# Optimization experiments

Hardware: AMD Instinct MI355X
Metric: run time of the kernel (lower is better)

Reference implementation:

```python
import jax, jax.numpy as jnp
import numpy as np

EMBED_DIM = 1024
NUM_HEADS = 16
HEAD_DIM = EMBED_DIM // NUM_HEADS


def setup_inputs() -> dict:
    key = jax.random.key(0)
    ks = jax.random.split(key, 11)
    Lq, N, E = 4096, 4, EMBED_DIM
    Lk = 4096
    s = 1.0 / np.sqrt(E)
    return {
        "q": jax.random.normal(ks[0], (Lq, N, E), jnp.float32),
        "k": jax.random.normal(ks[1], (Lk, N, E), jnp.float32),
        "v": jax.random.normal(ks[2], (Lk, N, E), jnp.float32),
        "Wq": jax.random.normal(ks[3], (E, E), jnp.float32) * s,
        "bq": jnp.zeros((E,), jnp.float32),
        "Wk": jax.random.normal(ks[4], (E, E), jnp.float32) * s,
        "bk": jnp.zeros((E,), jnp.float32),
        "Wv": jax.random.normal(ks[5], (E, E), jnp.float32) * s,
        "bv": jnp.zeros((E,), jnp.float32),
        "Wo": jax.random.normal(ks[6], (E, E), jnp.float32) * s,
        "bo": jnp.zeros((E,), jnp.float32),
    }


def reference(q, k, v, Wq, bq, Wk, bk, Wv, bv, Wo, bo):
    Lq, N, E = q.shape
    Lk = k.shape[0]
    H, D = NUM_HEADS, HEAD_DIM
    # Linear projections (torch Linear: x @ W.T + b)
    qp = q @ Wq.T + bq  # [Lq, N, E]
    kp = k @ Wk.T + bk  # [Lk, N, E]
    vp = v @ Wv.T + bv  # [Lk, N, E]
    # Split heads -> [N, H, L, D]
    qh = qp.reshape(Lq, N, H, D).transpose(1, 2, 0, 3)
    kh = kp.reshape(Lk, N, H, D).transpose(1, 2, 0, 3)
    vh = vp.reshape(Lk, N, H, D).transpose(1, 2, 0, 3)
    # Efficient (linear) attention
    kh = jax.nn.softmax(kh, axis=-2)            # softmax over sequence (L)
    v_prime = jnp.einsum('nhld,nhle->nhde', kh, vh)  # [N,H,D,D]
    qh = jax.nn.softmax(qh, axis=-1)            # softmax over feature (D)
    attn = jnp.einsum('nhld,nhde->nhle', qh, v_prime)  # [N,H,Lq,D]
    out = attn.transpose(2, 0, 1, 3).reshape(Lq, N, E)
    out = out @ Wo.T + bo
    return out
```

## Files before the change

kernel.cpp:

```cpp
#include <hip/hip_runtime.h>

typedef unsigned short u16;
typedef short s8v __attribute__((ext_vector_type(8)));
typedef float f4v __attribute__((ext_vector_type(4)));

#define D_LQ 4096
#define D_N 4
#define D_E 1024
#define D_M 16384
#define D_COLS 4096

__device__ __forceinline__ u16 f2b(float f) {
  unsigned u = __float_as_uint(f);
  return (u16)((u + 0x7FFFu + ((u >> 16) & 1u)) >> 16);
}
__device__ __forceinline__ float b2f(u16 x) {
  return __uint_as_float(((unsigned)x) << 16);
}
__device__ __forceinline__ s8v cvt8(float4 a, float4 b) {
  s8v o;
  o[0] = (short)f2b(a.x); o[1] = (short)f2b(a.y);
  o[2] = (short)f2b(a.z); o[3] = (short)f2b(a.w);
  o[4] = (short)f2b(b.x); o[5] = (short)f2b(b.y);
  o[6] = (short)f2b(b.z); o[7] = (short)f2b(b.w);
  return o;
}
__device__ __forceinline__ void gl_lds16(const void* g, void* l) {
  __builtin_amdgcn_global_load_lds(
      (const __attribute__((address_space(1))) void*)g,
      (__attribute__((address_space(3))) void*)l, 16, 0, 0);
}

__global__ void cvt_bf16(const float* __restrict__ in, u16* __restrict__ out, long n8) {
  long i = (long)blockIdx.x * 256 + threadIdx.x;
  if (i >= n8) return;
  const float4* p = (const float4*)in + 2 * i;
  float4 a = p[0], b = p[1];
  *(s8v*)(out + i * 8) = cvt8(a, b);
}

__global__ void cvt_w4(const float* __restrict__ W0, const float* __restrict__ W1,
                       const float* __restrict__ W2, const float* __restrict__ W3,
                       u16* __restrict__ O0, u16* __restrict__ O1,
                       u16* __restrict__ O2, u16* __restrict__ O3) {
  long i = (long)blockIdx.x * 256 + threadIdx.x;
  int w = blockIdx.y;
  const float* W = (w == 0) ? W0 : (w == 1) ? W1 : (w == 2) ? W2 : W3;
  u16* O = (w == 0) ? O0 : (w == 1) ? O1 : (w == 2) ? O2 : O3;
  const float4* p = (const float4*)W + 2 * i;
  float4 a = p[0], b = p[1];
  *(s8v*)(O + i * 8) = cvt8(a, b);
}

__global__ __launch_bounds__(256)
void gemm_bfb(const u16* __restrict__ A, const u16* __restrict__ B,
              const float* __restrict__ bias, u16* __restrict__ C) {
  __shared__ u16 As[128 * 32];
  __shared__ u16 Bs[128 * 32];
  const int tid = threadIdx.x;
  const int lane = tid & 63, r15 = lane & 15, khi = lane >> 4;
  const int wave = tid >> 6, wm = wave >> 1, wn = wave & 1;
  const int wg = blockIdx.y * 8 + blockIdx.x;
  const int xcd = wg & 7, j = wg >> 3;
  const int by = xcd * 16 + (j >> 3);
  const int bx = j & 7;
  f4v acc[4][4] = {};
  const u16* a0 = A + (long)(by * 128 + (tid >> 2)) * D_E + (tid & 3) * 8;
  const u16* b0 = B + (long)(bx * 128 + (tid >> 2)) * D_E + (tid & 3) * 8;
  const long rstep = (long)64 * D_E;
  u16* lA = As + tid * 8;
  u16* lB = Bs + tid * 8;
  for (int kt = 0; kt < D_E; kt += 32) {
    __syncthreads();
    gl_lds16(a0 + kt, lA);
    gl_lds16(a0 + rstep + kt, lA + 2048);
    gl_lds16(b0 + kt, lB);
    gl_lds16(b0 + rstep + kt, lB + 2048);
    __syncthreads();
    s8v af[4], bf[4];
#pragma unroll
    for (int m = 0; m < 4; m++)
      af[m] = *(const s8v*)(As + (wm * 64 + m * 16 + r15) * 32 + khi * 8);
#pragma unroll
    for (int n = 0; n < 4; n++)
      bf[n] = *(const s8v*)(Bs + (wn * 64 + n * 16 + r15) * 32 + khi * 8);
#pragma unroll
    for (int m = 0; m < 4; m++)
#pragma unroll
      for (int n = 0; n < 4; n++)
        acc[m][n] = __builtin_amdgcn_mfma_f32_16x16x32_bf16(af[m], bf[n], acc[m][n], 0, 0, 0);
  }
#pragma unroll
  for (int m = 0; m < 4; m++) {
    const int row = by * 128 + wm * 64 + m * 16 + khi * 4;
#pragma unroll
    for (int n = 0; n < 4; n++) {
      const int col = bx * 128 + wn * 64 + n * 16 + r15;
      const float bb = bias[col];
#pragma unroll
      for (int j2 = 0; j2 < 4; j2++)
        C[(long)(row + j2) * D_E + col] = f2b(acc[m][n][j2] + bb);
    }
  }
}

__global__ __launch_bounds__(256)
void gemm_bf_qsm(const u16* __restrict__ A, const u16* __restrict__ B,
                 const float* __restrict__ bias, u16* __restrict__ Csm) {
  __shared__ u16 As[128 * 32];
  __shared__ u16 Bs[128 * 32];
  const int tid = threadIdx.x;
  const int lane = tid & 63, r15 = lane & 15, khi = lane >> 4;
  const int wave = tid >> 6, wm = wave >> 1, wn = wave & 1;
  const int wg = blockIdx.y * 8 + blockIdx.x;
  const int xcd = wg & 7, j = wg >> 3;
  const int by = xcd * 16 + (j >> 3);
  const int bx = j & 7;
  f4v acc[4][4] = {};
  const u16* a0 = A + (long)(by * 128 + (tid >> 2)) * D_E + (tid & 3) * 8;
  const u16* b0 = B + (long)(bx * 128 + (tid >> 2)) * D_E + (tid & 3) * 8;
  const long rstep = (long)64 * D_E;
  u16* lA = As + tid * 8;
  u16* lB = Bs + tid * 8;
  for (int kt = 0; kt < D_E; kt += 32) {
    __syncthreads();
    gl_lds16(a0 + kt, lA);
    gl_lds16(a0 + rstep + kt, lA + 2048);
    gl_lds16(b0 + kt, lB);
    gl_lds16(b0 + rstep + kt, lB + 2048);
    __syncthreads();
    s8v af[4], bf[4];
#pragma unroll
    for (int m = 0; m < 4; m++)
      af[m] = *(const s8v*)(As + (wm * 64 + m * 16 + r15) * 32 + khi * 8);
#pragma unroll
    for (int n = 0; n < 4; n++)
      bf[n] = *(const s8v*)(Bs + (wn * 64 + n * 16 + r15) * 32 + khi * 8);
#pragma unroll
    for (int m = 0; m < 4; m++)
#pragma unroll
      for (int n = 0; n < 4; n++)
        acc[m][n] = __builtin_amdgcn_mfma_f32_16x16x32_bf16(af[m], bf[n], acc[m][n], 0, 0, 0);
  }
  const int colb = bx * 128 + wn * 64;
  float bb[4];
#pragma unroll
  for (int n = 0; n < 4; n++) bb[n] = bias[colb + n * 16 + r15];
#pragma unroll
  for (int m = 0; m < 4; m++) {
    const int row = by * 128 + wm * 64 + m * 16 + khi * 4;
#pragma unroll
    for (int j2 = 0; j2 < 4; j2++) {
      float e[4], s = 0.f;
#pragma unroll
      for (int n = 0; n < 4; n++) { e[n] = __expf(acc[m][n][j2] + bb[n]); s += e[n]; }
      s += __shfl_xor(s, 1);
      s += __shfl_xor(s, 2);
      s += __shfl_xor(s, 4);
      s += __shfl_xor(s, 8);
      float rs = 1.f / s;
#pragma unroll
      for (int n = 0; n < 4; n++)
        Csm[(long)(row + j2) * D_E + colb + n * 16 + r15] = f2b(e[n] * rs);
    }
  }
}

__global__ void k_sum(const u16* __restrict__ kb, float* __restrict__ psum) {
  int col = blockIdx.x * 256 + threadIdx.x;
  const u16* p = kb + (long)blockIdx.y * 64 * D_COLS + col;
  float s = 0.f;
  for (int l = 0; l < 64; l++) s += __expf(b2f(p[(long)l * D_COLS]));
  psum[blockIdx.y * D_COLS + col] = s;
}

__global__ void k_combine(const float* __restrict__ psum, float* __restrict__ crs) {
  int col = blockIdx.x * 256 + threadIdx.x;
  float s = 0.f;
  for (int i = 0; i < 64; i++) s += psum[i * D_COLS + col];
  crs[col] = 1.f / s;
}

__global__ __launch_bounds__(256)
void vprime_part(const u16* __restrict__ kw, const u16* __restrict__ vp,
                 const float* __restrict__ crs, float* __restrict__ part) {
  __shared__ float Ks[64 * 64];
  __shared__ float Vs[64 * 64];
  __shared__ float crS[64];
  int g = blockIdx.x, lc = blockIdx.y;
  int n = g >> 4, h = g & 15;
  int tid = threadIdx.x;
  int dt = (tid >> 4) * 4, et = (tid & 15) * 4;
  int r = tid >> 2, c16 = (tid & 3) * 16;
  if (tid < 64) crS[tid] = crs[n * D_E + h * 64 + tid];
  float acc[4][4] = {};
  long base = (long)lc * 512 * D_COLS + n * D_E + h * 64;
  for (int ch = 0; ch < 8; ch++) {
    long off = base + (long)(ch * 64 + r) * D_COLS + c16;
    __syncthreads();
#pragma unroll
    for (int qq = 0; qq < 16; qq++) {
      Ks[r * 64 + c16 + qq] = __expf(b2f(kw[off + qq])) * crS[c16 + qq];
      Vs[r * 64 + c16 + qq] = b2f(vp[off + qq]);
    }
    __syncthreads();
    for (int l = 0; l < 64; l++) {
      float kf[4], vf[4];
#pragma unroll
      for (int i = 0; i < 4; i++) { kf[i] = Ks[l * 64 + dt + i]; vf[i] = Vs[l * 64 + et + i]; }
#pragma unroll
      for (int i = 0; i < 4; i++)
#pragma unroll
        for (int j = 0; j < 4; j++) acc[i][j] += kf[i] * vf[j];
    }
  }
#pragma unroll
  for (int i = 0; i < 4; i++)
#pragma unroll
    for (int j = 0; j < 4; j++)
      part[(((long)lc * 64 + g) * 64 + (dt + i)) * 64 + et + j] = acc[i][j];
}

__global__ void vprime_red(const float* __restrict__ part, u16* __restrict__ vpb) {
  long id = (long)blockIdx.x * 256 + threadIdx.x;
  float s = 0.f;
  for (int lc = 0; lc < 8; lc++) s += part[(long)lc * 64 * 4096 + id];
  vpb[id] = f2b(s);
}

__global__ __launch_bounds__(256)
void u_mfma(const u16* __restrict__ Wob, const u16* __restrict__ vpb,
            u16* __restrict__ Ub) {
  __shared__ u16 Qs[128 * 64];
  __shared__ u16 Ps[64 * 64];
  const int ot = blockIdx.x, g = blockIdx.y;
  const int nb = g >> 4, h = g & 15;
  const int tid = threadIdx.x;
  const int lane = tid & 63, r15 = lane & 15, khi = lane >> 4;
  const int w = tid >> 6;
#pragma unroll
  for (int it = 0; it < 4; it++) {
    int c = it * 256 + tid;
    int row = c >> 3, cb = (c & 7) * 16;
    int swz = cb ^ ((row & 7) << 4);
    gl_lds16(Wob + (long)(ot * 128 + row) * D_E + h * 64 + (swz >> 1), Qs + c * 8);
  }
#pragma unroll
  for (int it = 0; it < 2; it++) {
    int c = it * 256 + tid;
    int row = c >> 3, cb = (c & 7) * 16;
    int swz = cb ^ ((row & 7) << 4);
    gl_lds16(vpb + ((long)g << 12) + row * 64 + (swz >> 1), Ps + c * 8);
  }
  __syncthreads();
  f4v acc[2][4] = {};
#pragma unroll
  for (int ks = 0; ks < 2; ks++) {
    s8v af[2], bf[4];
#pragma unroll
    for (int mf = 0; mf < 2; mf++) {
      int row = w * 32 + mf * 16 + r15;
      int boff = row * 128 + ((ks * 64 + khi * 16) ^ ((row & 7) << 4));
      af[mf] = *(const s8v*)((const char*)Qs + boff);
    }
#pragma unroll
    for (int nf = 0; nf < 4; nf++) {
      int row = nf * 16 + r15;
      int boff = row * 128 + ((ks * 64 + khi * 16) ^ ((row & 7) << 4));
      bf[nf] = *(const s8v*)((const char*)Ps + boff);
    }
#pragma unroll
    for (int mf = 0; mf < 2; mf++)
#pragma unroll
      for (int nf = 0; nf < 4; nf++)
        acc[mf][nf] = __builtin_amdgcn_mfma_f32_16x16x32_bf16(af[mf], bf[nf], acc[mf][nf], 0, 0, 0);
  }
#pragma unroll
  for (int mf = 0; mf < 2; mf++) {
#pragma unroll
    for (int nf = 0; nf < 4; nf++) {
#pragma unroll
      for (int j = 0; j < 4; j++) {
        int o = ot * 128 + w * 32 + mf * 16 + khi * 4 + j;
        int d = nf * 16 + r15;
        Ub[((long)nb * 1024 + o) * 1024 + h * 64 + d] = f2b(acc[mf][nf][j]);
      }
    }
  }
}

__global__ __launch_bounds__(256)
void gemm_out(const u16* __restrict__ Aq, const u16* __restrict__ Bu,
              const float* __restrict__ bias, float* __restrict__ C) {
  __shared__ u16 As[128 * 32];
  __shared__ u16 Bs[128 * 32];
  const int tid = threadIdx.x;
  const int lane = tid & 63, r15 = lane & 15, khi = lane >> 4;
  const int wave = tid >> 6, wm = wave >> 1, wn = wave & 1;
  const int n = blockIdx.z;
  const int wg = blockIdx.y * 8 + blockIdx.x;
  const int xcd = wg & 7, j = wg >> 3;
  const int by = xcd * 4 + (j >> 3);
  const int bx = j & 7;
  f4v acc[4][4] = {};
  const u16* a0 = Aq + ((long)(by * 128 + (tid >> 2)) * 4 + n) * D_E + (tid & 3) * 8;
  const u16* b0 = Bu + ((long)n * 1024 + bx * 128 + (tid >> 2)) * D_E + (tid & 3) * 8;
  const long rstepA = (long)64 * 4 * D_E;
  const long rstepB = (long)64 * D_E;
  u16* lA = As + tid * 8;
  u16* lB = Bs + tid * 8;
  for (int kt = 0; kt < D_E; kt += 32) {
    __syncthreads();
    gl_lds16(a0 + kt, lA);
    gl_lds16(a0 + rstepA + kt, lA + 2048);
    gl_lds16(b0 + kt, lB);
    gl_lds16(b0 + rstepB + kt, lB + 2048);
    __syncthreads();
    s8v af[4], bf[4];
#pragma unroll
    for (int m = 0; m < 4; m++)
      af[m] = *(const s8v*)(As + (wm * 64 + m * 16 + r15) * 32 + khi * 8);
#pragma unroll
    for (int nn = 0; nn < 4; nn++)
      bf[nn] = *(const s8v*)(Bs + (wn * 64 + nn * 16 + r15) * 32 + khi * 8);
#pragma unroll
    for (int m = 0; m < 4; m++)
#pragma unroll
      for (int nn = 0; nn < 4; nn++)
        acc[m][nn] = __builtin_amdgcn_mfma_f32_16x16x32_bf16(af[m], bf[nn], acc[m][nn], 0, 0, 0);
  }
#pragma unroll
  for (int m = 0; m < 4; m++) {
    const int row = by * 128 + wm * 64 + m * 16 + khi * 4;
#pragma unroll
    for (int nn = 0; nn < 4; nn++) {
      const int col = bx * 128 + wn * 64 + nn * 16 + r15;
      const float bb = bias[col];
#pragma unroll
      for (int j2 = 0; j2 < 4; j2++)
        C[((long)(row + j2) * 4 + n) * D_E + col] = acc[m][nn][j2] + bb;
    }
  }
}

__global__ void sentinel(float* __restrict__ out, int wsbad) {
  if (blockIdx.x == 0 && threadIdx.x == 0 && wsbad) {
    out[0] += 100.0f;
  }
}

extern "C" void kernel_launch(void* const* d_in, const int* in_sizes, int n_in,
                              void* d_out, int out_size, void* d_ws, size_t ws_size,
                              hipStream_t stream) {
  const float* q  = (const float*)d_in[0];
  const float* k  = (const float*)d_in[1];
  const float* v  = (const float*)d_in[2];
  const float* Wq = (const float*)d_in[3];
  const float* bq = (const float*)d_in[4];
  const float* Wk = (const float*)d_in[5];
  const float* bk = (const float*)d_in[6];
  const float* Wv = (const float*)d_in[7];
  const float* bv = (const float*)d_in[8];
  const float* Wo = (const float*)d_in[9];
  const float* bo = (const float*)d_in[10];

  char* ws = (char*)d_ws;
  size_t off = 0;
  u16* kb; u16* vb; float* psum; float* crs; float* part; u16* vpb;
  u16* xb; u16* Wqb; u16* Wkb; u16* Wvb; u16* Wob; u16* Ub;
  kb   = (u16*)(ws + off);   off += (size_t)D_M * D_E * 2;
  vb   = (u16*)(ws + off);   off += (size_t)D_M * D_E * 2;
  psum = (float*)(ws + off); off += (size_t)64 * D_COLS * 4;
  crs  = (float*)(ws + off); off += (size_t)D_COLS * 4;
  part = (float*)(ws + off); off += (size_t)8 * 64 * 4096 * 4;
  vpb  = (u16*)(ws + off);   off += (size_t)64 * 4096 * 2;
  xb   = (u16*)(ws + off);   off += (size_t)D_M * D_E * 2;
  Wqb  = (u16*)(ws + off);   off += (size_t)D_E * D_E * 2;
  Wkb  = (u16*)(ws + off);   off += (size_t)D_E * D_E * 2;
  Wvb  = (u16*)(ws + off);   off += (size_t)D_E * D_E * 2;
  Wob  = (u16*)(ws + off);   off += (size_t)D_E * D_E * 2;
  Ub   = (u16*)(ws + off);   off += (size_t)4 * 1024 * 1024 * 2;
  size_t need = off;
  u16* qsm = kb;
  int wsbad = (ws_size < need) ? 1 : 0;

  const long nX8 = (long)D_M * D_E / 8;
  const long nW8 = (long)D_E * D_E / 8;
  dim3 blk(256);
  dim3 ggrid(D_E / 128, D_M / 128);

  cvt_w4<<<dim3(nW8 / 256, 4), blk, 0, stream>>>(Wq, Wk, Wv, Wo, Wqb, Wkb, Wvb, Wob);

  cvt_bf16<<<dim3(nX8 / 256), blk, 0, stream>>>(k, xb, nX8);
  gemm_bfb<<<ggrid, blk, 0, stream>>>(xb, Wkb, bk, kb);
  cvt_bf16<<<dim3(nX8 / 256), blk, 0, stream>>>(v, xb, nX8);
  gemm_bfb<<<ggrid, blk, 0, stream>>>(xb, Wvb, bv, vb);

  k_sum<<<dim3(16, 64), blk, 0, stream>>>(kb, psum);
  k_combine<<<dim3(16), blk, 0, stream>>>(psum, crs);

  vprime_part<<<dim3(64, 8), blk, 0, stream>>>(kb, vb, crs, part);
  vprime_red<<<dim3(64 * 4096 / 256), blk, 0, stream>>>(part, vpb);

  u_mfma<<<dim3(8, 64), blk, 0, stream>>>(Wob, vpb, Ub);

  cvt_bf16<<<dim3(nX8 / 256), blk, 0, stream>>>(q, xb, nX8);
  gemm_bf_qsm<<<ggrid, blk, 0, stream>>>(xb, Wqb, bq, qsm);

  gemm_out<<<dim3(8, 32, 4), blk, 0, stream>>>(qsm, Ub, bo, (float*)d_out);

  sentinel<<<dim3(1), dim3(64), 0, stream>>>((float*)d_out, wsbad);
}
```

Measured before the change: 325.6 us.

## Replace 128x128 GEMMs with pipelined 256x256 triple-buffered swizzled-LDS GEMM template

Replaces the four separate 128x128-tile GEMM kernels with one templated 256x256-tile kernel using 512 threads. It triple-buffers LDS, prefetches two k-steps ahead via global_load_lds with explicit vmcnt waits, and XOR-swizzles the LDS layout to avoid bank conflicts. The MFMA work is split into two halves around the prefetch issue and wrapped with setprio. The goal is to hide global-load latency and raise data reuse per tile, at the cost of more LDS and registers per block and fewer blocks in flight.

```diff
diff --git a/kernel.cpp b/kernel.cpp
--- a/kernel.cpp
+++ b/kernel.cpp
@@ -30,6 +30,13 @@
       (const __attribute__((address_space(1))) void*)g,
       (__attribute__((address_space(3))) void*)l, 16, 0, 0);
 }
+__device__ __forceinline__ void barr() {
+  asm volatile("" ::: "memory");
+  __builtin_amdgcn_s_barrier();
+  asm volatile("" ::: "memory");
+}
+#define WAITV4 asm volatile("s_waitcnt vmcnt(4)" ::: "memory")
+#define WAITV0 asm volatile("s_waitcnt vmcnt(0)" ::: "memory")
 
 __global__ void cvt_bf16(const float* __restrict__ in, u16* __restrict__ out, long n8) {
   long i = (long)blockIdx.x * 256 + threadIdx.x;
@@ -52,117 +59,135 @@
   *(s8v*)(O + i * 8) = cvt8(a, b);
 }
 
-__global__ __launch_bounds__(256)
-void gemm_bfb(const u16* __restrict__ A, const u16* __restrict__ B,
-              const float* __restrict__ bias, u16* __restrict__ C) {
-  __shared__ u16 As[128 * 32];
-  __shared__ u16 Bs[128 * 32];
+__device__ __forceinline__ void stage256(const u16* __restrict__ src0, long rstride,
+                                         u16* __restrict__ lds, int tid) {
+#pragma unroll
+  for (int L = 0; L < 2; L++) {
+    int g = tid + L * 512;
+    int row = g >> 2, c = g & 3;
+    int sc = c ^ ((row ^ (row >> 2)) & 3);
+    gl_lds16(src0 + (long)row * rstride + sc * 8, lds + g * 8);
+  }
+}
+__device__ __forceinline__ s8v fr(const u16* __restrict__ lds, int row, int khi) {
+  return *(const s8v*)(lds + row * 32 + ((khi ^ ((row ^ (row >> 2)) & 3)) * 8));
+}
+
+template <int EPI, bool STRIDED>
+__global__ __launch_bounds__(512, 2)
+void gemm256(const u16* __restrict__ A, const u16* __restrict__ B,
+             const float* __restrict__ bias, void* __restrict__ Cv) {
+  __shared__ u16 As[3][256 * 32];
+  __shared__ u16 Bs[3][256 * 32];
   const int tid = threadIdx.x;
   const int lane = tid & 63, r15 = lane & 15, khi = lane >> 4;
-  const int wave = tid >> 6, wm = wave >> 1, wn = wave & 1;
-  const int wg = blockIdx.y * 8 + blockIdx.x;
-  const int xcd = wg & 7, j = wg >> 3;
-  const int by = xcd * 16 + (j >> 3);
-  const int bx = j & 7;
-  f4v acc[4][4] = {};
-  const u16* a0 = A + (long)(by * 128 + (tid >> 2)) * D_E + (tid & 3) * 8;
-  const u16* b0 = B + (long)(bx * 128 + (tid >> 2)) * D_E + (tid & 3) * 8;
-  const long rstep = (long)64 * D_E;
-  u16* lA = As + tid * 8;
-  u16* lB = Bs + tid * 8;
-  for (int kt = 0; kt < D_E; kt += 32) {
-    __syncthreads();
-    gl_lds16(a0 + kt, lA);
-    gl_lds16(a0 + rstep + kt, lA + 2048);
-    gl_lds16(b0 + kt, lB);
-    gl_lds16(b0 + rstep + kt, lB + 2048);
-    __syncthreads();
-    s8v af[4], bf[4];
-#pragma unroll
-    for (int m = 0; m < 4; m++)
-      af[m] = *(const s8v*)(As + (wm * 64 + m * 16 + r15) * 32 + khi * 8);
-#pragma unroll
-    for (int n = 0; n < 4; n++)
-      bf[n] = *(const s8v*)(Bs + (wn * 64 + n * 16 + r15) * 32 + khi * 8);
-#pragma unroll
-    for (int m = 0; m < 4; m++)
-#pragma unroll
-      for (int n = 0; n < 4; n++)
-        acc[m][n] = __builtin_amdgcn_mfma_f32_16x16x32_bf16(af[m], bf[n], acc[m][n], 0, 0, 0);
-  }
-#pragma unroll
-  for (int m = 0; m < 4; m++) {
-    const int row = by * 128 + wm * 64 + m * 16 + khi * 4;
-#pragma unroll
-    for (int n = 0; n < 4; n++) {
-      const int col = bx * 128 + wn * 64 + n * 16 + r15;
-      const float bb = bias[col];
-#pragma unroll
-      for (int j2 = 0; j2 < 4; j2++)
-        C[(long)(row + j2) * D_E + col] = f2b(acc[m][n][j2] + bb);
-    }
-  }
-}
-
-__global__ __launch_bounds__(256)
-void gemm_bf_qsm(const u16* __restrict__ A, const u16* __restrict__ B,
-                 const float* __restrict__ bias, u16* __restrict__ Csm) {
-  __shared__ u16 As[128 * 32];
-  __shared__ u16 Bs[128 * 32];
-  const int tid = threadIdx.x;
-  const int lane = tid & 63, r15 = lane & 15, khi = lane >> 4;
-  const int wave = tid >> 6, wm = wave >> 1, wn = wave & 1;
-  const int wg = blockIdx.y * 8 + blockIdx.x;
-  const int xcd = wg & 7, j = wg >> 3;
-  const int by = xcd * 16 + (j >> 3);
-  const int bx = j & 7;
-  f4v acc[4][4] = {};
-  const u16* a0 = A + (long)(by * 128 + (tid >> 2)) * D_E + (tid & 3) * 8;
-  const u16* b0 = B + (long)(bx * 128 + (tid >> 2)) * D_E + (tid & 3) * 8;
-  const long rstep = (long)64 * D_E;
-  u16* lA = As + tid * 8;
-  u16* lB = Bs + tid * 8;
-  for (int kt = 0; kt < D_E; kt += 32) {
-    __syncthreads();
-    gl_lds16(a0 + kt, lA);
-    gl_lds16(a0 + rstep + kt, lA + 2048);
-    gl_lds16(b0 + kt, lB);
-    gl_lds16(b0 + rstep + kt, lB + 2048);
-    __syncthreads();
-    s8v af[4], bf[4];
-#pragma unroll
-    for (int m = 0; m < 4; m++)
-      af[m] = *(const s8v*)(As + (wm * 64 + m * 16 + r15) * 32 + khi * 8);
-#pragma unroll
-    for (int n = 0; n < 4; n++)
-      bf[n] = *(const s8v*)(Bs + (wn * 64 + n * 16 + r15) * 32 + khi * 8);
-#pragma unroll
-    for (int m = 0; m < 4; m++)
-#pragma unroll
-      for (int n = 0; n < 4; n++)
-        acc[m][n] = __builtin_amdgcn_mfma_f32_16x16x32_bf16(af[m], bf[n], acc[m][n], 0, 0, 0);
-  }
-  const int colb = bx * 128 + wn * 64;
-  float bb[4];
-#pragma unroll
-  for (int n = 0; n < 4; n++) bb[n] = bias[colb + n * 16 + r15];
-#pragma unroll
-  for (int m = 0; m < 4; m++) {
-    const int row = by * 128 + wm * 64 + m * 16 + khi * 4;
-#pragma unroll
-    for (int j2 = 0; j2 < 4; j2++) {
-      float e[4], s = 0.f;
-#pragma unroll
-      for (int n = 0; n < 4; n++) { e[n] = __expf(acc[m][n][j2] + bb[n]); s += e[n]; }
-      s += __shfl_xor(s, 1);
-      s += __shfl_xor(s, 2);
-      s += __shfl_xor(s, 4);
-      s += __shfl_xor(s, 8);
-      float rs = 1.f / s;
-#pragma unroll
-      for (int n = 0; n < 4; n++)
-        Csm[(long)(row + j2) * D_E + colb + n * 16 + r15] = f2b(e[n] * rs);
-    }
+  const int w = tid >> 6, wm = w >> 2, wn = w & 3;
+  int gg = STRIDED ? (int)((blockIdx.z * gridDim.y + blockIdx.y) * gridDim.x + blockIdx.x)
+                   : (int)(blockIdx.y * gridDim.x + blockIdx.x);
+  int s = (gg & 7) * 32 + (gg >> 3);
+  int zn, by, bx;
+  if (STRIDED) { zn = s >> 6; by = (s >> 2) & 15; bx = s & 3; }
+  else         { zn = 0;      by = s >> 2;        bx = s & 3; }
+  const long arst = STRIDED ? 4096 : 1024;
+  const u16* abase = STRIDED ? (A + ((long)(by * 256) * 4 + zn) * 1024)
+                             : (A + (long)(by * 256) * 1024);
+  const u16* bbase = B + ((STRIDED ? (long)zn * 1024 : 0) + bx * 256) * 1024;
+
+  stage256(abase + 0, arst, As[0], tid);
+  stage256(bbase + 0, 1024, Bs[0], tid);
+  stage256(abase + 32, arst, As[1], tid);
+  stage256(bbase + 32, 1024, Bs[1], tid);
+  WAITV4;
+  barr();
+
+  f4v acc[8][4] = {};
+#pragma unroll 1
+  for (int t = 0; t < 32; t++) {
+    const u16* as = As[t % 3];
+    const u16* bs = Bs[t % 3];
+    s8v bfr[4], afr[4];
+#pragma unroll
+    for (int nf = 0; nf < 4; nf++) bfr[nf] = fr(bs, wn * 64 + nf * 16 + r15, khi);
+#pragma unroll
+    for (int i = 0; i < 4; i++) afr[i] = fr(as, wm * 128 + i * 16 + r15, khi);
+    if (t < 30) stage256(abase + (t + 2) * 32, arst, As[(t + 2) % 3], tid);
+    barr();
+    __builtin_amdgcn_s_setprio(1);
+#pragma unroll
+    for (int i = 0; i < 4; i++)
+#pragma unroll
+      for (int nf = 0; nf < 4; nf++)
+        acc[i][nf] = __builtin_amdgcn_mfma_f32_16x16x32_bf16(afr[i], bfr[nf], acc[i][nf], 0, 0, 0);
+    __builtin_amdgcn_s_setprio(0);
+    barr();
+#pragma unroll
+    for (int i = 0; i < 4; i++) afr[i] = fr(as, wm * 128 + (i + 4) * 16 + r15, khi);
+    if (t < 30) stage256(bbase + (t + 2) * 32, 1024, Bs[(t + 2) % 3], tid);
+    barr();
+    __builtin_amdgcn_s_setprio(1);
+#pragma unroll
+    for (int i = 0; i < 4; i++)
+#pragma unroll
+      for (int nf = 0; nf < 4; nf++)
+        acc[i + 4][nf] = __builtin_amdgcn_mfma_f32_16x16x32_bf16(afr[i], bfr[nf], acc[i + 4][nf], 0, 0, 0);
+    __builtin_amdgcn_s_setprio(0);
+    if (t < 30) { WAITV4; } else { WAITV0; }
+    barr();
+  }
+
+  const int colb = bx * 256 + wn * 64;
+  const long rowb = (long)by * 256 + wm * 128;
+  if (EPI == 1) {
+    float bb[4];
+#pragma unroll
+    for (int nf = 0; nf < 4; nf++) bb[nf] = bias[colb + nf * 16 + r15];
+    u16* C = (u16*)Cv;
+#pragma unroll
+    for (int m = 0; m < 8; m++) {
+#pragma unroll
+      for (int j = 0; j < 4; j++) {
+        float e[4], ssum = 0.f;
+#pragma unroll
+        for (int nf = 0; nf < 4; nf++) { e[nf] = __expf(acc[m][nf][j] + bb[nf]); ssum += e[nf]; }
+        ssum += __shfl_xor(ssum, 1);
+        ssum += __shfl_xor(ssum, 2);
+        ssum += __shfl_xor(ssum, 4);
+        ssum += __shfl_xor(ssum, 8);
+        float rs = 1.f / ssum;
+        long row = rowb + m * 16 + khi * 4 + j;
+#pragma unroll
+        for (int nf = 0; nf < 4; nf++)
+          C[row * 1024 + colb + nf * 16 + r15] = f2b(e[nf] * rs);
+      }
+    }
+  } else if (EPI == 0) {
+    u16* C = (u16*)Cv;
+#pragma unroll
+    for (int m = 0; m < 8; m++)
+#pragma unroll
+      for (int nf = 0; nf < 4; nf++) {
+        int col = colb + nf * 16 + r15;
+        float bb = bias[col];
+#pragma unroll
+        for (int j = 0; j < 4; j++) {
+          long row = rowb + m * 16 + khi * 4 + j;
+          C[row * 1024 + col] = f2b(acc[m][nf][j] + bb);
+        }
+      }
+  } else {
+    float* C = (float*)Cv;
+#pragma unroll
+    for (int m = 0; m < 8; m++)
+#pragma unroll
+      for (int nf = 0; nf < 4; nf++) {
+        int col = colb + nf * 16 + r15;
+        float bb = bias[col];
+#pragma unroll
+        for (int j = 0; j < 4; j++) {
+          long row = rowb + m * 16 + khi * 4 + j;
+          C[(row * 4 + zn) * 1024 + col] = acc[m][nf][j] + bb;
+        }
+      }
   }
 }
 
@@ -285,60 +310,6 @@
         int d = nf * 16 + r15;
         Ub[((long)nb * 1024 + o) * 1024 + h * 64 + d] = f2b(acc[mf][nf][j]);
       }
-    }
-  }
-}
-
-__global__ __launch_bounds__(256)
-void gemm_out(const u16* __restrict__ Aq, const u16* __restrict__ Bu,
-              const float* __restrict__ bias, float* __restrict__ C) {
-  __shared__ u16 As[128 * 32];
-  __shared__ u16 Bs[128 * 32];
-  const int tid = threadIdx.x;
-  const int lane = tid & 63, r15 = lane & 15, khi = lane >> 4;
-  const int wave = tid >> 6, wm = wave >> 1, wn = wave & 1;
-  const int n = blockIdx.z;
-  const int wg = blockIdx.y * 8 + blockIdx.x;
-  const int xcd = wg & 7, j = wg >> 3;
-  const int by = xcd * 4 + (j >> 3);
-  const int bx = j & 7;
-  f4v acc[4][4] = {};
-  const u16* a0 = Aq + ((long)(by * 128 + (tid >> 2)) * 4 + n) * D_E + (tid & 3) * 8;
-  const u16* b0 = Bu + ((long)n * 1024 + bx * 128 + (tid >> 2)) * D_E + (tid & 3) * 8;
-  const long rstepA = (long)64 * 4 * D_E;
-  const long rstepB = (long)64 * D_E;
-  u16* lA = As + tid * 8;
-  u16* lB = Bs + tid * 8;
-  for (int kt = 0; kt < D_E; kt += 32) {
-    __syncthreads();
-    gl_lds16(a0 + kt, lA);
-    gl_lds16(a0 + rstepA + kt, lA + 2048);
-    gl_lds16(b0 + kt, lB);
-    gl_lds16(b0 + rstepB + kt, lB + 2048);
-    __syncthreads();
-    s8v af[4], bf[4];
-#pragma unroll
-    for (int m = 0; m < 4; m++)
-      af[m] = *(const s8v*)(As + (wm * 64 + m * 16 + r15) * 32 + khi * 8);
-#pragma unroll
-    for (int nn = 0; nn < 4; nn++)
-      bf[nn] = *(const s8v*)(Bs + (wn * 64 + nn * 16 + r15) * 32 + khi * 8);
-#pragma unroll
-    for (int m = 0; m < 4; m++)
-#pragma unroll
-      for (int nn = 0; nn < 4; nn++)
-        acc[m][nn] = __builtin_amdgcn_mfma_f32_16x16x32_bf16(af[m], bf[nn], acc[m][nn], 0, 0, 0);
-  }
-#pragma unroll
-  for (int m = 0; m < 4; m++) {
-    const int row = by * 128 + wm * 64 + m * 16 + khi * 4;
-#pragma unroll
-    for (int nn = 0; nn < 4; nn++) {
-      const int col = bx * 128 + wn * 64 + nn * 16 + r15;
-      const float bb = bias[col];
-#pragma unroll
-      for (int j2 = 0; j2 < 4; j2++)
-        C[((long)(row + j2) * 4 + n) * D_E + col] = acc[m][nn][j2] + bb;
     }
   }
 }
@@ -387,14 +358,14 @@
   const long nX8 = (long)D_M * D_E / 8;
   const long nW8 = (long)D_E * D_E / 8;
   dim3 blk(256);
-  dim3 ggrid(D_E / 128, D_M / 128);
+  dim3 blk5(512);
 
   cvt_w4<<<dim3(nW8 / 256, 4), blk, 0, stream>>>(Wq, Wk, Wv, Wo, Wqb, Wkb, Wvb, Wob);
 
   cvt_bf16<<<dim3(nX8 / 256), blk, 0, stream>>>(k, xb, nX8);
-  gemm_bfb<<<ggrid, blk, 0, stream>>>(xb, Wkb, bk, kb);
+  gemm256<0, false><<<dim3(4, 64), blk5, 0, stream>>>(xb, Wkb, bk, (void*)kb);
   cvt_bf16<<<dim3(nX8 / 256), blk, 0, stream>>>(v, xb, nX8);
-  gemm_bfb<<<ggrid, blk, 0, stream>>>(xb, Wvb, bv, vb);
+  gemm256<0, false><<<dim3(4, 64), blk5, 0, stream>>>(xb, Wvb, bv, (void*)vb);
 
   k_sum<<<dim3(16, 64), blk, 0, stream>>>(kb, psum);
   k_combine<<<dim3(16), blk, 0, stream>>>(psum, crs);
@@ -405,9 +376,9 @@
   u_mfma<<<dim3(8, 64), blk, 0, stream>>>(Wob, vpb, Ub);
 
   cvt_bf16<<<dim3(nX8 / 256), blk, 0, stream>>>(q, xb, nX8);
-  gemm_bf_qsm<<<ggrid, blk, 0, stream>>>(xb, Wqb, bq, qsm);
-
-  gemm_out<<<dim3(8, 32, 4), blk, 0, stream>>>(qsm, Ub, bo, (float*)d_out);
+  gemm256<1, false><<<dim3(4, 64), blk5, 0, stream>>>(xb, Wqb, bq, (void*)qsm);
+
+  gemm256<2, true><<<dim3(4, 16, 4), blk5, 0, stream>>>(qsm, Ub, bo, d_out);
 
   sentinel<<<dim3(1), dim3(64), 0, stream>>>((float*)d_out, wsbad);
 }
```

Measured after the change: 295.3 us. 1.1x faster.
